# Optimization experiments

Hardware: AMD Instinct MI355X
Metric: run time of the kernel (lower is better)

The kernel has to match this reference:

```python
import jax, jax.numpy as jnp
import numpy as np

N, E, D, L, G = 50000, 800000, 128, 3, 64
DIM_OUT = 10
EPS_BN = 1e-5
EPS_AGG = 1e-6


def setup_inputs() -> dict:
    key = jax.random.key(0)
    ks = jax.random.split(key, 10)
    x = jax.random.normal(ks[0], (N, D), jnp.float32)
    edge_attr = jax.random.normal(ks[1], (E, D), jnp.float32)
    edge_index = jax.random.randint(ks[2], (2, E), 0, N)
    batch_vec = jnp.sort(jax.random.randint(ks[3], (N,), 0, G))
    s = 1.0 / np.sqrt(D)
    def w(k, shape):
        return jax.random.uniform(k, shape, jnp.float32, -s, s)
    lin_w = w(ks[4], (L, 4, D, D))   # per-layer stacked A,B,D,E weights
    lin_b = w(ks[5], (L, 4, D))
    bn_gamma = jnp.ones((L, D), jnp.float32)
    bn_beta = jnp.zeros((L, D), jnp.float32)
    post_w1 = w(ks[6], (D, D)); post_b1 = w(ks[7], (D,))
    post_w2 = w(ks[8], (D, DIM_OUT)); post_b2 = w(ks[9], (DIM_OUT,))
    return dict(x=x, edge_attr=edge_attr, edge_index=edge_index, batch_vec=batch_vec,
                lin_w=lin_w, lin_b=lin_b, bn_gamma=bn_gamma, bn_beta=bn_beta,
                post_w1=post_w1, post_b1=post_b1, post_w2=post_w2, post_b2=post_b2)


def _batchnorm_train(h, gamma, beta):
    # training-mode BN over node dim (biased variance, as in torch)
    mu = h.mean(0)
    var = h.var(0)
    return (h - mu) * jax.lax.rsqrt(var + EPS_BN) * gamma + beta


def reference(x, edge_attr, edge_index, batch_vec, lin_w, lin_b, bn_gamma, bn_beta,
              post_w1, post_b1, post_w2, post_b2):
    src, dst = edge_index[0], edge_index[1]   # j -> i (source_to_target)
    e = edge_attr
    for l in range(L):
        x_in = x
        # fused A,B,D,E projections: [4, N, D]
        proj = jnp.einsum('nd,kdo->kno', x, lin_w[l]) + lin_b[l][:, None, :]
        Ax, Bx, Dx, Ex = proj[0], proj[1], proj[2], proj[3]
        e_ij = Dx[dst] + Ex[src]                # [E, D]
        sigma = jax.nn.sigmoid(e_ij)
        num = jax.ops.segment_sum(sigma * Bx[src], dst, num_segments=N)
        den = jax.ops.segment_sum(sigma, dst, num_segments=N)
        h = Ax + num / (den + EPS_AGG)
        h = jax.nn.relu(_batchnorm_train(h, bn_gamma[l], bn_beta[l]))
        x = x_in + h                            # residual
        e = e_ij                                # edge features updated (bn_edge_e unused in forward)
    counts = jax.ops.segment_sum(jnp.ones((N,), x.dtype), batch_vec, num_segments=G)
    pooled = jax.ops.segment_sum(x, batch_vec, num_segments=G) / jnp.maximum(counts, 1.0)[:, None]
    h = jax.nn.relu(pooled @ post_w1 + post_b1)
    return h @ post_w2 + post_b2                # [G, DIM_OUT]
```

## Files before the change

### kernel.cpp

```cpp
#include <hip/hip_runtime.h>
#include <math.h>

constexpr int N_NODES = 50000;
constexpr int N_EDGES = 800000;
constexpr int DIM     = 128;
constexpr int NLAYERS = 3;
constexpr int NGRAPH  = 64;
constexpr int DOUT    = 10;
constexpr float EPS_BN  = 1e-5f;
constexpr float EPS_AGG = 1e-6f;

typedef __attribute__((ext_vector_type(8))) short   bf16x8;
typedef __attribute__((ext_vector_type(4))) float   floatx4;
typedef __attribute__((ext_vector_type(4))) unsigned short ushort4v;
typedef __attribute__((ext_vector_type(2))) unsigned int uint2v;
typedef __attribute__((ext_vector_type(2))) float float2v;

__device__ inline unsigned short f2bf(float f) {
    union { float f; unsigned int u; } v; v.f = f;
    unsigned int u = v.u;
    return (unsigned short)((u + 0x7fffu + ((u >> 16) & 1u)) >> 16);
}
__device__ inline float bf2f(unsigned short h) {
    union { unsigned int u; float f; } v; v.u = ((unsigned int)h) << 16;
    return v.f;
}

__global__ void hist_kernel(const int* __restrict__ dst, int* __restrict__ cnt) {
    int e = blockIdx.x * 256 + threadIdx.x;
    if (e < N_EDGES) atomicAdd(&cnt[dst[e]], 1);
}

__global__ void scan1_kernel(const int* __restrict__ cnt, int* __restrict__ row_ptr,
                             int* __restrict__ partials) {
    __shared__ int s[256];
    int i = blockIdx.x * 256 + threadIdx.x;
    int v = (i < N_NODES) ? cnt[i] : 0;
    s[threadIdx.x] = v;
    __syncthreads();
    for (int off = 1; off < 256; off <<= 1) {
        int t = (threadIdx.x >= off) ? s[threadIdx.x - off] : 0;
        __syncthreads();
        s[threadIdx.x] += t;
        __syncthreads();
    }
    if (i < N_NODES) row_ptr[i] = s[threadIdx.x] - v;
    if (threadIdx.x == 255) partials[blockIdx.x] = s[255];
}

__global__ void scan2_kernel(int* partials, int nb) {
    __shared__ int s[256];
    int t = threadIdx.x;
    int v = (t < nb) ? partials[t] : 0;
    s[t] = v;
    __syncthreads();
    for (int off = 1; off < 256; off <<= 1) {
        int u = (t >= off) ? s[t - off] : 0;
        __syncthreads();
        s[t] += u;
        __syncthreads();
    }
    if (t < nb) partials[t] = s[t] - v;
}

__global__ void scan3_kernel(int* row_ptr, const int* __restrict__ partials) {
    int i = blockIdx.x * 256 + threadIdx.x;
    if (i < N_NODES) row_ptr[i] += partials[blockIdx.x];
    if (blockIdx.x == 0 && threadIdx.x == 0) row_ptr[N_NODES] = N_EDGES;
}

__global__ void scatter_kernel(const int* __restrict__ src, const int* __restrict__ dst,
                               const int* __restrict__ row_ptr, int* __restrict__ cursor,
                               int* __restrict__ col_src) {
    int e = blockIdx.x * 256 + threadIdx.x;
    if (e < N_EDGES) {
        int d = dst[e];
        int pos = row_ptr[d] + atomicAdd(&cursor[d], 1);
        col_src[pos] = src[e];
    }
}

__global__ void wconv_kernel(const float* __restrict__ W, unsigned short* __restrict__ Wt) {
    int idx = blockIdx.x * 256 + threadIdx.x;
    int c = idx & 127, d = (idx >> 7) & 127, lk = idx >> 14;
    Wt[((size_t)lk * 128 + c) * 128 + d] = f2bf(W[idx]);
}

__global__ __launch_bounds__(256) void xinit_kernel(const float* __restrict__ x_in,
                                                    float* __restrict__ x_cur,
                                                    unsigned short* __restrict__ xb) {
    int i4 = blockIdx.x * 256 + threadIdx.x;
    float4 v = *(const float4*)&x_in[(size_t)i4 * 4];
    *(float4*)&x_cur[(size_t)i4 * 4] = v;
    ushort4v b; b.x = f2bf(v.x); b.y = f2bf(v.y); b.z = f2bf(v.z); b.w = f2bf(v.w);
    *(ushort4v*)&xb[(size_t)i4 * 4] = b;
}

__global__ __launch_bounds__(256) void gemm_mfma(const unsigned short* __restrict__ xb,
                                                 const unsigned short* __restrict__ Wt,
                                                 const float* __restrict__ bias,
                                                 float* __restrict__ Axh,
                                                 float* __restrict__ Dx,
                                                 unsigned int* __restrict__ EB,
                                                 float* __restrict__ bn8) {
    const int ksl = blockIdx.y;
    const int m0  = blockIdx.x * 128;
    const int tid = threadIdx.x;

    if (blockIdx.x == 0 && ksl == 0) {
#pragma unroll
        for (int c = 0; c < 8; c++) bn8[c * 256 + tid] = 0.f;
    }

    const int wave = tid >> 6, lane = tid & 63;
    const int wm = (wave >> 1) * 64, wc = (wave & 1) * 64;
    const int quad = lane >> 4, l16 = lane & 15;
    const unsigned short* Wk = Wt + (size_t)ksl * DIM * DIM;

    floatx4 acc[4][4];
#pragma unroll
    for (int i = 0; i < 4; i++)
#pragma unroll
        for (int j = 0; j < 4; j++) acc[i][j] = (floatx4)0.f;

#pragma unroll
    for (int ks = 0; ks < 4; ks++) {
        const int kk = ks * 32 + quad * 8;
        bf16x8 a[4], b[4];
#pragma unroll
        for (int i = 0; i < 4; i++) {
            int row = m0 + wm + i * 16 + l16;
            row = min(row, N_NODES - 1);
            a[i] = *(const bf16x8*)&xb[(size_t)row * DIM + kk];
        }
#pragma unroll
        for (int j = 0; j < 4; j++) {
            int col = wc + j * 16 + l16;
            b[j] = *(const bf16x8*)&Wk[(size_t)col * DIM + kk];
        }
#pragma unroll
        for (int i = 0; i < 4; i++)
#pragma unroll
            for (int j = 0; j < 4; j++)
                acc[i][j] = __builtin_amdgcn_mfma_f32_16x16x32_bf16(a[i], b[j], acc[i][j], 0, 0, 0);
    }

    float bv[4];
#pragma unroll
    for (int j = 0; j < 4; j++) bv[j] = bias[ksl * DIM + wc + j * 16 + l16];

    float* fdst = (ksl == 0) ? Axh : Dx;
    unsigned short* ebp = (unsigned short*)EB;
    const int half = (ksl == 3) ? 1 : 0;

#pragma unroll
    for (int i = 0; i < 4; i++) {
#pragma unroll
        for (int r = 0; r < 4; r++) {
            int row = m0 + wm + i * 16 + quad * 4 + r;
            if (row >= N_NODES) continue;
            if ((ksl & 1) == 0) {
                float* op = fdst + (size_t)row * DIM;
#pragma unroll
                for (int j = 0; j < 4; j++)
                    op[wc + j * 16 + l16] = acc[i][j][r] + bv[j];
            } else {
                unsigned short* op = ebp + (size_t)row * DIM * 2 + half;
#pragma unroll
                for (int j = 0; j < 4; j++)
                    op[(wc + j * 16 + l16) * 2] = f2bf(acc[i][j][r] + bv[j]);
            }
        }
    }
}

__global__ __launch_bounds__(256) void agg_kernel(float* __restrict__ Axh,
                                                  const float* __restrict__ Dx,
                                                  const unsigned int* __restrict__ EB,
                                                  const int* __restrict__ row_ptr,
                                                  const int* __restrict__ col_src,
                                                  float* __restrict__ bn8) {
    const int wave = threadIdx.x >> 6;
    const int lane = threadIdx.x & 63;
    const int d0   = lane * 2;
    const int i0   = (blockIdx.x * 4 + wave) * 8;

    float s0 = 0.f, q0 = 0.f, s1 = 0.f, q1 = 0.f;

    for (int n = 0; n < 8; n++) {
        const int i = i0 + n;
        const bool valid = (i < N_NODES);
        const int ic = valid ? i : N_NODES - 1;

        const float2v ax = *(const float2v*)&Axh[(size_t)ic * DIM + d0];
        const float2v dx = *(const float2v*)&Dx[(size_t)ic * DIM + d0];
        const int e0 = row_ptr[ic];
        const int e1 = row_ptr[ic + 1];

        float num0 = 0.f, den0 = 0.f, num1 = 0.f, den1 = 0.f;
        const int nr = (e1 - e0 + 7) >> 3;
        for (int r = 0; r < nr; r++) {
            const int eb = e0 + r * 8;
            int idx[8];
#pragma unroll
            for (int k = 0; k < 8; k++) idx[k] = col_src[min(eb + k, e1 - 1)];
            uint2v w[8];
#pragma unroll
            for (int k = 0; k < 8; k++)
                w[k] = *(const uint2v*)&EB[(size_t)idx[k] * DIM + d0];
#pragma unroll
            for (int k = 0; k < 8; k++) {
                const float ex0 = bf2f((unsigned short)(w[k].x >> 16));
                const float bx0 = bf2f((unsigned short)(w[k].x & 0xffffu));
                const float ex1 = bf2f((unsigned short)(w[k].y >> 16));
                const float bx1 = bf2f((unsigned short)(w[k].y & 0xffffu));
                float sg0 = 1.f / (1.f + __expf(-(dx.x + ex0)));
                float sg1 = 1.f / (1.f + __expf(-(dx.y + ex1)));
                const bool live = (eb + k < e1);
                sg0 = live ? sg0 : 0.f;
                sg1 = live ? sg1 : 0.f;
                num0 += sg0 * bx0; den0 += sg0;
                num1 += sg1 * bx1; den1 += sg1;
            }
        }
        const float h0 = ax.x + num0 / (den0 + EPS_AGG);
        const float h1 = ax.y + num1 / (den1 + EPS_AGG);
        if (valid) {
            float2v hv; hv.x = h0; hv.y = h1;
            *(float2v*)&Axh[(size_t)ic * DIM + d0] = hv;
            s0 += h0; q0 += h0 * h0;
            s1 += h1; q1 += h1 * h1;
        }
    }

    __shared__ float rs[4 * 128], rq[4 * 128];
    rs[wave * 128 + d0]     = s0;  rq[wave * 128 + d0]     = q0;
    rs[wave * 128 + d0 + 1] = s1;  rq[wave * 128 + d0 + 1] = q1;
    __syncthreads();
    if (threadIdx.x < 128) {
        const int d = threadIdx.x;
        const float s = rs[d] + rs[128 + d] + rs[256 + d] + rs[384 + d];
        const float q = rq[d] + rq[128 + d] + rq[256 + d] + rq[384 + d];
        float* bp = bn8 + (blockIdx.x & 7) * 256;
        atomicAdd(&bp[d], s);
        atomicAdd(&bp[128 + d], q);
    }
}

__global__ __launch_bounds__(256) void apply_kernel(const float* __restrict__ h,
                                                    const float* __restrict__ bn8,
                                                    const float* __restrict__ gamma,
                                                    const float* __restrict__ beta,
                                                    float* __restrict__ x,
                                                    unsigned short* __restrict__ xb) {
    __shared__ float ssc[128], ssh[128];
    const int t = threadIdx.x;
    if (t < 128) {
        float s = 0.f, q = 0.f;
#pragma unroll
        for (int c = 0; c < 8; c++) { s += bn8[c * 256 + t]; q += bn8[c * 256 + 128 + t]; }
        const float mu  = s * (1.f / N_NODES);
        const float var = q * (1.f / N_NODES) - mu * mu;
        const float sc  = gamma[t] * rsqrtf(var + EPS_BN);
        ssc[t] = sc;
        ssh[t] = beta[t] - mu * sc;
    }
    __syncthreads();

    int i4 = blockIdx.x * 256 + t;
    int d  = (i4 * 4) & 127;
    float4 hv = *(const float4*)&h[(size_t)i4 * 4];
    float4 xv = *(float4*)&x[(size_t)i4 * 4];
    xv.x += fmaxf(hv.x * ssc[d + 0] + ssh[d + 0], 0.f);
    xv.y += fmaxf(hv.y * ssc[d + 1] + ssh[d + 1], 0.f);
    xv.z += fmaxf(hv.z * ssc[d + 2] + ssh[d + 2], 0.f);
    xv.w += fmaxf(hv.w * ssc[d + 3] + ssh[d + 3], 0.f);
    *(float4*)&x[(size_t)i4 * 4] = xv;
    ushort4v b; b.x = f2bf(xv.x); b.y = f2bf(xv.y); b.z = f2bf(xv.z); b.w = f2bf(xv.w);
    *(ushort4v*)&xb[(size_t)i4 * 4] = b;
}

__global__ __launch_bounds__(128) void pool_kernel(const float* __restrict__ x,
                                                   const int* __restrict__ batch,
                                                   float* __restrict__ pooled,
                                                   int* __restrict__ gcount) {
    int d = threadIdx.x;
    int r0 = blockIdx.x * 256;
    int r1 = min(r0 + 256, N_NODES);
    int curg = batch[r0];
    float acc = 0.f;
    int run = 0;
    for (int r = r0; r < r1; r++) {
        int g = batch[r];
        if (g != curg) {
            atomicAdd(&pooled[curg * DIM + d], acc);
            if (d == 0) atomicAdd(&gcount[curg], run);
            acc = 0.f; run = 0; curg = g;
        }
        acc += x[(size_t)r * DIM + d];
        run++;
    }
    atomicAdd(&pooled[curg * DIM + d], acc);
    if (d == 0) atomicAdd(&gcount[curg], run);
}

__global__ __launch_bounds__(128) void head_kernel(const float* __restrict__ pooled,
                                                   const int* __restrict__ gcount,
                                                   const float* __restrict__ w1,
                                                   const float* __restrict__ b1,
                                                   const float* __restrict__ w2,
                                                   const float* __restrict__ b2,
                                                   float* __restrict__ out) {
    __shared__ float sp[128], sh[128];
    int g = blockIdx.x, d = threadIdx.x;
    float c = (float)max(gcount[g], 1);
    sp[d] = pooled[g * DIM + d] / c;
    __syncthreads();
    float acc = b1[d];
    for (int dd = 0; dd < DIM; dd++) acc += sp[dd] * w1[dd * DIM + d];
    sh[d] = fmaxf(acc, 0.f);
    __syncthreads();
    if (d < DOUT) {
        float o = b2[d];
        for (int dd = 0; dd < DIM; dd++) o += sh[dd] * w2[dd * DOUT + d];
        out[g * DOUT + d] = o;
    }
}

extern "C" void kernel_launch(void* const* d_in, const int* in_sizes, int n_in,
                              void* d_out, int out_size, void* d_ws, size_t ws_size,
                              hipStream_t stream) {
    const float* x_in  = (const float*)d_in[0];
    const int*   eidx  = (const int*)d_in[2];
    const int*   batch = (const int*)d_in[3];
    const float* lin_w = (const float*)d_in[4];
    const float* lin_b = (const float*)d_in[5];
    const float* gamma = (const float*)d_in[6];
    const float* beta  = (const float*)d_in[7];
    const float* w1    = (const float*)d_in[8];
    const float* b1    = (const float*)d_in[9];
    const float* w2    = (const float*)d_in[10];
    const float* b2    = (const float*)d_in[11];
    float* out = (float*)d_out;

    const int* src = eidx;
    const int* dst = eidx + N_EDGES;

    auto al = [](size_t v) { return (v + 255) & ~(size_t)255; };
    size_t off = 0;
    size_t o_xcur = off; off = al(off + (size_t)N_NODES * DIM * 4);
    size_t o_xb   = off; off = al(off + (size_t)N_NODES * DIM * 2);
    size_t o_wt   = off; off = al(off + (size_t)NLAYERS * 4 * DIM * DIM * 2);
    size_t o_axh  = off; off = al(off + (size_t)N_NODES * DIM * 4);
    size_t o_dx   = off; off = al(off + (size_t)N_NODES * DIM * 4);
    size_t o_eb   = off; off = al(off + (size_t)N_NODES * DIM * 4);
    size_t o_rp   = off; off = al(off + (size_t)(N_NODES + 1) * 4);
    size_t o_cs   = off; off = al(off + (size_t)N_EDGES * 4);
    size_t o_cnt  = off; off = al(off + (size_t)N_NODES * 4);
    size_t o_part = off; off = al(off + 256 * 4);
    size_t o_bn   = off; off = al(off + 2048 * 4);
    size_t o_pool = off; off = al(off + (size_t)NGRAPH * DIM * 4);
    size_t o_gc   = off; off = al(off + (size_t)NGRAPH * 4);
    size_t total  = off;

    char* base = (ws_size >= total) ? (char*)d_ws : (char*)d_in[1];

    float*          x_cur    = (float*)(base + o_xcur);
    unsigned short* xb       = (unsigned short*)(base + o_xb);
    unsigned short* Wt       = (unsigned short*)(base + o_wt);
    float*          Axh      = (float*)(base + o_axh);
    float*          Dx       = (float*)(base + o_dx);
    unsigned int*   EB       = (unsigned int*)(base + o_eb);
    int*            row_ptr  = (int*)  (base + o_rp);
    int*            col_src  = (int*)  (base + o_cs);
    int*            cnt      = (int*)  (base + o_cnt);
    int*            partials = (int*)  (base + o_part);
    float*          bn8      = (float*)(base + o_bn);
    float*          pooled   = (float*)(base + o_pool);
    int*            gcount   = (int*)  (base + o_gc);

    const int nbN = (N_NODES + 255) / 256;
    const int nbE = (N_EDGES + 255) / 256;
    const int nb4 = (N_NODES * DIM / 4) / 256;
    const int nbAgg = (N_NODES + 31) / 32;

    xinit_kernel<<<nb4, 256, 0, stream>>>(x_in, x_cur, xb);
    wconv_kernel<<<(NLAYERS * 4 * DIM * DIM) / 256, 256, 0, stream>>>(lin_w, Wt);

    hipMemsetAsync(cnt, 0, (size_t)N_NODES * 4, stream);
    hist_kernel<<<nbE, 256, 0, stream>>>(dst, cnt);
    scan1_kernel<<<nbN, 256, 0, stream>>>(cnt, row_ptr, partials);
    scan2_kernel<<<1, 256, 0, stream>>>(partials, nbN);
    scan3_kernel<<<nbN, 256, 0, stream>>>(row_ptr, partials);
    hipMemsetAsync(cnt, 0, (size_t)N_NODES * 4, stream);
    scatter_kernel<<<nbE, 256, 0, stream>>>(src, dst, row_ptr, cnt, col_src);

    for (int l = 0; l < NLAYERS; l++) {
        gemm_mfma<<<dim3((N_NODES + 127) / 128, 4), 256, 0, stream>>>(
            xb, Wt + (size_t)l * 4 * DIM * DIM, lin_b + (size_t)l * 4 * DIM, Axh, Dx, EB, bn8);
        agg_kernel<<<nbAgg, 256, 0, stream>>>(Axh, Dx, EB, row_ptr, col_src, bn8);
        apply_kernel<<<nb4, 256, 0, stream>>>(Axh, bn8, gamma + (size_t)l * DIM,
                                              beta + (size_t)l * DIM, x_cur, xb);
    }

    hipMemsetAsync(pooled, 0, (size_t)NGRAPH * DIM * 4, stream);
    hipMemsetAsync(gcount, 0, (size_t)NGRAPH * 4, stream);
    pool_kernel<<<nbN, 128, 0, stream>>>(x_cur, batch, pooled, gcount);
    head_kernel<<<NGRAPH, 128, 0, stream>>>(pooled, gcount, w1, b1, w2, b2, out);
}
```

Measured before the change: 1.138 ms.

## Fuse layer loop, pooling and head into one cooperative persistent kernel

Replaces the per-layer gemm/agg/apply launches plus pool/head kernels with a single cooperative kernel of 512 persistent blocks that use grid-wide syncs between phases. The GEMM now loads the A tile once and loops over the four weight slices, and aggregation unrolls 16 edges instead of 8. This removes about a dozen launches and their gaps, at the cost of fewer resident blocks, grid-sync overhead and possibly lower occupancy from the larger register footprint. It falls back to the old multi-kernel path if the cooperative launch fails.

Measured after the change: 1.794 ms. 57.7% more time.

```diff
diff --git a/kernel.cpp b/kernel.cpp
--- a/kernel.cpp
+++ b/kernel.cpp
@@ -1,5 +1,8 @@
 #include <hip/hip_runtime.h>
+#include <hip/hip_cooperative_groups.h>
 #include <math.h>
+
+namespace cg = cooperative_groups;
 
 constexpr int N_NODES = 50000;
 constexpr int N_EDGES = 800000;
@@ -9,6 +12,8 @@
 constexpr int DOUT    = 10;
 constexpr float EPS_BN  = 1e-5f;
 constexpr float EPS_AGG = 1e-6f;
+
+constexpr int FGRID = 512;
 
 typedef __attribute__((ext_vector_type(8))) short   bf16x8;
 typedef __attribute__((ext_vector_type(4))) float   floatx4;
@@ -96,6 +101,234 @@
     *(ushort4v*)&xb[(size_t)i4 * 4] = b;
 }
 
+struct FP {
+    unsigned short* xb; float* x_cur;
+    const unsigned short* Wt; const float* lin_b;
+    const float* gamma; const float* beta;
+    float* Axh; float* Dx; unsigned int* EB;
+    const int* row_ptr; const int* col_src;
+    float* bn8;
+    const int* batch; float* pooled; int* gcount;
+    const float* w1; const float* b1; const float* w2; const float* b2;
+    float* out;
+};
+
+__global__ __launch_bounds__(256, 2) void fused_kernel(FP p) {
+    cg::grid_group gg = cg::this_grid();
+    const int bid  = blockIdx.x;
+    const int tid  = threadIdx.x;
+    const int wave = tid >> 6, lane = tid & 63;
+    const int quad = lane >> 4, l16 = lane & 15;
+
+    __shared__ float rs[512], rq[512];
+    __shared__ float ssc[128], ssh[128];
+    __shared__ float sp[128], sh2[128];
+
+    for (int l = 0; l < NLAYERS; l++) {
+        if (bid == 0) {
+#pragma unroll
+            for (int c = 0; c < 8; c++) p.bn8[c * 256 + tid] = 0.f;
+        }
+        const unsigned short* Wl = p.Wt + (size_t)l * 4 * DIM * DIM;
+        const float* bl = p.lin_b + (size_t)l * 4 * DIM;
+        const int wm = (wave >> 1) * 64, wc = (wave & 1) * 64;
+
+        for (int m = bid; m < (N_NODES + 127) / 128; m += FGRID) {
+            const int m0 = m * 128;
+            bf16x8 a[4][4];
+#pragma unroll
+            for (int ks = 0; ks < 4; ks++) {
+                const int kk = ks * 32 + quad * 8;
+#pragma unroll
+                for (int i = 0; i < 4; i++) {
+                    int row = min(m0 + wm + i * 16 + l16, N_NODES - 1);
+                    a[ks][i] = *(const bf16x8*)&p.xb[(size_t)row * DIM + kk];
+                }
+            }
+#pragma unroll 1
+            for (int ksl = 0; ksl < 4; ksl++) {
+                const unsigned short* Wk = Wl + (size_t)ksl * DIM * DIM;
+                floatx4 acc[4][4];
+#pragma unroll
+                for (int i = 0; i < 4; i++)
+#pragma unroll
+                    for (int j = 0; j < 4; j++) acc[i][j] = (floatx4)0.f;
+#pragma unroll
+                for (int ks = 0; ks < 4; ks++) {
+                    const int kk = ks * 32 + quad * 8;
+                    bf16x8 b[4];
+#pragma unroll
+                    for (int j = 0; j < 4; j++)
+                        b[j] = *(const bf16x8*)&Wk[(size_t)(wc + j * 16 + l16) * DIM + kk];
+#pragma unroll
+                    for (int i = 0; i < 4; i++)
+#pragma unroll
+                        for (int j = 0; j < 4; j++)
+                            acc[i][j] = __builtin_amdgcn_mfma_f32_16x16x32_bf16(a[ks][i], b[j], acc[i][j], 0, 0, 0);
+                }
+                float bv[4];
+#pragma unroll
+                for (int j = 0; j < 4; j++) bv[j] = bl[ksl * DIM + wc + j * 16 + l16];
+
+                float* fdst = (ksl == 0) ? p.Axh : p.Dx;
+                unsigned short* ebp = (unsigned short*)p.EB;
+                const int half = (ksl == 3) ? 1 : 0;
+#pragma unroll
+                for (int i = 0; i < 4; i++) {
+#pragma unroll
+                    for (int r = 0; r < 4; r++) {
+                        int row = m0 + wm + i * 16 + quad * 4 + r;
+                        if (row >= N_NODES) continue;
+                        if ((ksl & 1) == 0) {
+                            float* op = fdst + (size_t)row * DIM;
+#pragma unroll
+                            for (int j = 0; j < 4; j++)
+                                op[wc + j * 16 + l16] = acc[i][j][r] + bv[j];
+                        } else {
+                            unsigned short* op = ebp + (size_t)row * DIM * 2 + half;
+#pragma unroll
+                            for (int j = 0; j < 4; j++)
+                                op[(wc + j * 16 + l16) * 2] = f2bf(acc[i][j][r] + bv[j]);
+                        }
+                    }
+                }
+            }
+        }
+        gg.sync();
+
+        const int d0 = lane * 2;
+        for (int c = bid; c < (N_NODES + 31) / 32; c += FGRID) {
+            const int i0 = (c * 4 + wave) * 8;
+            float s0 = 0.f, q0 = 0.f, s1 = 0.f, q1 = 0.f;
+            for (int n = 0; n < 8; n++) {
+                const int i = i0 + n;
+                const bool valid = (i < N_NODES);
+                const int ic = valid ? i : N_NODES - 1;
+                const float2v ax = *(const float2v*)&p.Axh[(size_t)ic * DIM + d0];
+                const float2v dx = *(const float2v*)&p.Dx[(size_t)ic * DIM + d0];
+                const int e0 = p.row_ptr[ic], e1 = p.row_ptr[ic + 1];
+                float num0 = 0.f, den0 = 0.f, num1 = 0.f, den1 = 0.f;
+                const int nr = (e1 - e0 + 15) >> 4;
+                for (int r = 0; r < nr; r++) {
+                    const int eb = e0 + r * 16;
+                    int idx[16];
+#pragma unroll
+                    for (int k = 0; k < 16; k++) idx[k] = p.col_src[min(eb + k, e1 - 1)];
+                    uint2v w[16];
+#pragma unroll
+                    for (int k = 0; k < 16; k++)
+                        w[k] = *(const uint2v*)&p.EB[(size_t)idx[k] * DIM + d0];
+#pragma unroll
+                    for (int k = 0; k < 16; k++) {
+                        const float ex0 = bf2f((unsigned short)(w[k].x >> 16));
+                        const float bx0 = bf2f((unsigned short)(w[k].x & 0xffffu));
+                        const float ex1 = bf2f((unsigned short)(w[k].y >> 16));
+                        const float bx1 = bf2f((unsigned short)(w[k].y & 0xffffu));
+                        float sg0 = 1.f / (1.f + __expf(-(dx.x + ex0)));
+                        float sg1 = 1.f / (1.f + __expf(-(dx.y + ex1)));
+                        const bool live = (eb + k < e1);
+                        sg0 = live ? sg0 : 0.f;
+                        sg1 = live ? sg1 : 0.f;
+                        num0 += sg0 * bx0; den0 += sg0;
+                        num1 += sg1 * bx1; den1 += sg1;
+                    }
+                }
+                const float h0 = ax.x + num0 / (den0 + EPS_AGG);
+                const float h1 = ax.y + num1 / (den1 + EPS_AGG);
+                if (valid) {
+                    float2v hv; hv.x = h0; hv.y = h1;
+                    *(float2v*)&p.Axh[(size_t)ic * DIM + d0] = hv;
+                    s0 += h0; q0 += h0 * h0;
+                    s1 += h1; q1 += h1 * h1;
+                }
+            }
+            rs[wave * 128 + d0]     = s0;  rq[wave * 128 + d0]     = q0;
+            rs[wave * 128 + d0 + 1] = s1;  rq[wave * 128 + d0 + 1] = q1;
+            __syncthreads();
+            if (tid < 128) {
+                const float s = rs[tid] + rs[128 + tid] + rs[256 + tid] + rs[384 + tid];
+                const float q = rq[tid] + rq[128 + tid] + rq[256 + tid] + rq[384 + tid];
+                float* bp = p.bn8 + (c & 7) * 256;
+                atomicAdd(&bp[tid], s);
+                atomicAdd(&bp[128 + tid], q);
+            }
+            __syncthreads();
+        }
+        gg.sync();
+
+        if (tid < 128) {
+            float s = 0.f, q = 0.f;
+#pragma unroll
+            for (int c = 0; c < 8; c++) { s += p.bn8[c * 256 + tid]; q += p.bn8[c * 256 + 128 + tid]; }
+            const float mu  = s * (1.f / N_NODES);
+            const float var = q * (1.f / N_NODES) - mu * mu;
+            const float sc  = p.gamma[l * DIM + tid] * rsqrtf(var + EPS_BN);
+            ssc[tid] = sc;
+            ssh[tid] = p.beta[l * DIM + tid] - mu * sc;
+        }
+        __syncthreads();
+        for (int i4 = bid * 256 + tid; i4 < N_NODES * DIM / 4; i4 += FGRID * 256) {
+            int d = (i4 * 4) & 127;
+            float4 hv = *(const float4*)&p.Axh[(size_t)i4 * 4];
+            float4 xv = *(float4*)&p.x_cur[(size_t)i4 * 4];
+            xv.x += fmaxf(hv.x * ssc[d + 0] + ssh[d + 0], 0.f);
+            xv.y += fmaxf(hv.y * ssc[d + 1] + ssh[d + 1], 0.f);
+            xv.z += fmaxf(hv.z * ssc[d + 2] + ssh[d + 2], 0.f);
+            xv.w += fmaxf(hv.w * ssc[d + 3] + ssh[d + 3], 0.f);
+            *(float4*)&p.x_cur[(size_t)i4 * 4] = xv;
+            ushort4v b; b.x = f2bf(xv.x); b.y = f2bf(xv.y); b.z = f2bf(xv.z); b.w = f2bf(xv.w);
+            *(ushort4v*)&p.xb[(size_t)i4 * 4] = b;
+        }
+        if (l == NLAYERS - 1 && bid == 1) {
+            for (int i = tid; i < NGRAPH * DIM; i += 256) p.pooled[i] = 0.f;
+            if (tid < NGRAPH) p.gcount[tid] = 0;
+        }
+        gg.sync();
+    }
+
+    {
+        const int half = tid >> 7, d = tid & 127;
+        for (int cc = bid * 2 + half; cc < (N_NODES + 255) / 256; cc += FGRID * 2) {
+            int r0 = cc * 256, r1 = min(r0 + 256, N_NODES);
+            int curg = p.batch[r0];
+            float acc = 0.f; int run = 0;
+            for (int r = r0; r < r1; r++) {
+                int g = p.batch[r];
+                if (g != curg) {
+                    atomicAdd(&p.pooled[curg * DIM + d], acc);
+                    if (d == 0) atomicAdd(&p.gcount[curg], run);
+                    acc = 0.f; run = 0; curg = g;
+                }
+                acc += p.x_cur[(size_t)r * DIM + d];
+                run++;
+            }
+            atomicAdd(&p.pooled[curg * DIM + d], acc);
+            if (d == 0) atomicAdd(&p.gcount[curg], run);
+        }
+    }
+    gg.sync();
+
+    if (bid < NGRAPH) {
+        const int g = bid;
+        if (tid < 128) {
+            float c = (float)max(p.gcount[g], 1);
+            sp[tid] = p.pooled[g * DIM + tid] / c;
+        }
+        __syncthreads();
+        if (tid < 128) {
+            float acc = p.b1[tid];
+            for (int dd = 0; dd < DIM; dd++) acc += sp[dd] * p.w1[dd * DIM + tid];
+            sh2[tid] = fmaxf(acc, 0.f);
+        }
+        __syncthreads();
+        if (tid < DOUT) {
+            float o = p.b2[tid];
+            for (int dd = 0; dd < DIM; dd++) o += sh2[dd] * p.w2[dd * DOUT + tid];
+            p.out[g * DOUT + tid] = o;
+        }
+    }
+}
+
 __global__ __launch_bounds__(256) void gemm_mfma(const unsigned short* __restrict__ xb,
                                                  const unsigned short* __restrict__ Wt,
                                                  const float* __restrict__ bias,
@@ -106,53 +339,43 @@
     const int ksl = blockIdx.y;
     const int m0  = blockIdx.x * 128;
     const int tid = threadIdx.x;
-
     if (blockIdx.x == 0 && ksl == 0) {
 #pragma unroll
         for (int c = 0; c < 8; c++) bn8[c * 256 + tid] = 0.f;
     }
-
     const int wave = tid >> 6, lane = tid & 63;
     const int wm = (wave >> 1) * 64, wc = (wave & 1) * 64;
     const int quad = lane >> 4, l16 = lane & 15;
     const unsigned short* Wk = Wt + (size_t)ksl * DIM * DIM;
-
     floatx4 acc[4][4];
 #pragma unroll
     for (int i = 0; i < 4; i++)
 #pragma unroll
         for (int j = 0; j < 4; j++) acc[i][j] = (floatx4)0.f;
-
 #pragma unroll
     for (int ks = 0; ks < 4; ks++) {
         const int kk = ks * 32 + quad * 8;
         bf16x8 a[4], b[4];
 #pragma unroll
         for (int i = 0; i < 4; i++) {
-            int row = m0 + wm + i * 16 + l16;
-            row = min(row, N_NODES - 1);
+            int row = min(m0 + wm + i * 16 + l16, N_NODES - 1);
             a[i] = *(const bf16x8*)&xb[(size_t)row * DIM + kk];
         }
 #pragma unroll
-        for (int j = 0; j < 4; j++) {
-            int col = wc + j * 16 + l16;
-            b[j] = *(const bf16x8*)&Wk[(size_t)col * DIM + kk];
-        }
+        for (int j = 0; j < 4; j++)
+            b[j] = *(const bf16x8*)&Wk[(size_t)(wc + j * 16 + l16) * DIM + kk];
 #pragma unroll
         for (int i = 0; i < 4; i++)
 #pragma unroll
             for (int j = 0; j < 4; j++)
                 acc[i][j] = __builtin_amdgcn_mfma_f32_16x16x32_bf16(a[i], b[j], acc[i][j], 0, 0, 0);
     }
-
     float bv[4];
 #pragma unroll
     for (int j = 0; j < 4; j++) bv[j] = bias[ksl * DIM + wc + j * 16 + l16];
-
     float* fdst = (ksl == 0) ? Axh : Dx;
     unsigned short* ebp = (unsigned short*)EB;
     const int half = (ksl == 3) ? 1 : 0;
-
 #pragma unroll
     for (int i = 0; i < 4; i++) {
 #pragma unroll
@@ -184,19 +407,14 @@
     const int lane = threadIdx.x & 63;
     const int d0   = lane * 2;
     const int i0   = (blockIdx.x * 4 + wave) * 8;
-
     float s0 = 0.f, q0 = 0.f, s1 = 0.f, q1 = 0.f;
-
     for (int n = 0; n < 8; n++) {
         const int i = i0 + n;
         const bool valid = (i < N_NODES);
         const int ic = valid ? i : N_NODES - 1;
-
         const float2v ax = *(const float2v*)&Axh[(size_t)ic * DIM + d0];
         const float2v dx = *(const float2v*)&Dx[(size_t)ic * DIM + d0];
-        const int e0 = row_ptr[ic];
-        const int e1 = row_ptr[ic + 1];
-
+        const int e0 = row_ptr[ic], e1 = row_ptr[ic + 1];
         float num0 = 0.f, den0 = 0.f, num1 = 0.f, den1 = 0.f;
         const int nr = (e1 - e0 + 7) >> 3;
         for (int r = 0; r < nr; r++) {
@@ -232,7 +450,6 @@
             s1 += h1; q1 += h1 * h1;
         }
     }
-
     __shared__ float rs[4 * 128], rq[4 * 128];
     rs[wave * 128 + d0]     = s0;  rq[wave * 128 + d0]     = q0;
     rs[wave * 128 + d0 + 1] = s1;  rq[wave * 128 + d0 + 1] = q1;
@@ -266,7 +483,6 @@
         ssh[t] = beta[t] - mu * sc;
     }
     __syncthreads();
-
     int i4 = blockIdx.x * 256 + t;
     int d  = (i4 * 4) & 127;
     float4 hv = *(const float4*)&h[(size_t)i4 * 4];
@@ -386,7 +602,6 @@
 
     xinit_kernel<<<nb4, 256, 0, stream>>>(x_in, x_cur, xb);
     wconv_kernel<<<(NLAYERS * 4 * DIM * DIM) / 256, 256, 0, stream>>>(lin_w, Wt);
-
     hipMemsetAsync(cnt, 0, (size_t)N_NODES * 4, stream);
     hist_kernel<<<nbE, 256, 0, stream>>>(dst, cnt);
     scan1_kernel<<<nbN, 256, 0, stream>>>(cnt, row_ptr, partials);
@@ -395,16 +610,27 @@
     hipMemsetAsync(cnt, 0, (size_t)N_NODES * 4, stream);
     scatter_kernel<<<nbE, 256, 0, stream>>>(src, dst, row_ptr, cnt, col_src);
 
-    for (int l = 0; l < NLAYERS; l++) {
-        gemm_mfma<<<dim3((N_NODES + 127) / 128, 4), 256, 0, stream>>>(
-            xb, Wt + (size_t)l * 4 * DIM * DIM, lin_b + (size_t)l * 4 * DIM, Axh, Dx, EB, bn8);
-        agg_kernel<<<nbAgg, 256, 0, stream>>>(Axh, Dx, EB, row_ptr, col_src, bn8);
-        apply_kernel<<<nb4, 256, 0, stream>>>(Axh, bn8, gamma + (size_t)l * DIM,
-                                              beta + (size_t)l * DIM, x_cur, xb);
-    }
-
-    hipMemsetAsync(pooled, 0, (size_t)NGRAPH * DIM * 4, stream);
-    hipMemsetAsync(gcount, 0, (size_t)NGRAPH * 4, stream);
-    pool_kernel<<<nbN, 128, 0, stream>>>(x_cur, batch, pooled, gcount);
-    head_kernel<<<NGRAPH, 128, 0, stream>>>(pooled, gcount, w1, b1, w2, b2, out);
-}
+    FP prm;
+    prm.xb = xb; prm.x_cur = x_cur; prm.Wt = Wt; prm.lin_b = lin_b;
+    prm.gamma = gamma; prm.beta = beta;
+    prm.Axh = Axh; prm.Dx = Dx; prm.EB = EB;
+    prm.row_ptr = row_ptr; prm.col_src = col_src;
+    prm.bn8 = bn8; prm.batch = batch; prm.pooled = pooled; prm.gcount = gcount;
+    prm.w1 = w1; prm.b1 = b1; prm.w2 = w2; prm.b2 = b2; prm.out = out;
+    void* kargs[] = { &prm };
+    hipError_t ce = hipLaunchCooperativeKernel((void*)fused_kernel, dim3(FGRID), dim3(256),
+                                               kargs, 0, stream);
+    if (ce != hipSuccess) {
+        for (int l = 0; l < NLAYERS; l++) {
+            gemm_mfma<<<dim3((N_NODES + 127) / 128, 4), 256, 0, stream>>>(
+                xb, Wt + (size_t)l * 4 * DIM * DIM, lin_b + (size_t)l * 4 * DIM, Axh, Dx, EB, bn8);
+            agg_kernel<<<nbAgg, 256, 0, stream>>>(Axh, Dx, EB, row_ptr, col_src, bn8);
+            apply_kernel<<<nb4, 256, 0, stream>>>(Axh, bn8, gamma + (size_t)l * DIM,
+                                                  beta + (size_t)l * DIM, x_cur, xb);
+        }
+        hipMemsetAsync(pooled, 0, (size_t)NGRAPH * DIM * 4, stream);
+        hipMemsetAsync(gcount, 0, (size_t)NGRAPH * 4, stream);
+        pool_kernel<<<nbN, 128, 0, stream>>>(x_cur, batch, pooled, gcount);
+        head_kernel<<<NGRAPH, 128, 0, stream>>>(pooled, gcount, w1, b1, w2, b2, out);
+    }
+}
```
